# Kernel tuning notes

Measured on AMD Instinct MI355X. Metric: run time of the kernel, lower is better.

## Reference

```python
import jax, jax.numpy as jnp
import numpy as np

HYP_C = 0.1
TAU = 0.1
MRG = 0.1
CLIP_R = 2.3
BS = 1024
NB_PROXIES = 256
SZ_EMBED = 128
T_BATCH = BS * 50
T_LCA = NB_PROXIES * 50


@jax.custom_vjp
def artanh(x):
    xc = jnp.clip(x, -1.0 + 1e-5, 1.0 - 1e-5)
    return 0.5 * (jnp.log1p(xc) - jnp.log1p(-xc))

def _artanh_fwd(x):
    xc = jnp.clip(x, -1.0 + 1e-5, 1.0 - 1e-5)
    return 0.5 * (jnp.log1p(xc) - jnp.log1p(-xc)), xc

def _artanh_bwd(xc, g):
    return (g / (1.0 - xc * xc),)

artanh.defvjp(_artanh_fwd, _artanh_bwd)


@jax.custom_vjp
def riemannian_fix(x):
    # identity fwd; bwd rescales euclidean grad to riemannian grad on the ball
    return x

def _riem_fwd(x):
    return x, x

def _riem_bwd(x, g):
    scale = ((1.0 - HYP_C * jnp.sum(x * x, axis=-1, keepdims=True)) ** 2) / 4.0
    return (g * scale,)

riemannian_fix.defvjp(_riem_fwd, _riem_bwd)


def expmap0(x, c):
    sqrt_c = c ** 0.5
    xn = jnp.maximum(jnp.linalg.norm(x, axis=-1, keepdims=True), 1e-5)
    return jnp.tanh(sqrt_c * xn) * x / (sqrt_c * xn)


def project(x, c):
    norm = jnp.maximum(jnp.linalg.norm(x, axis=-1, keepdims=True), 1e-5)
    maxnorm = (1.0 - 1e-3) / (c ** 0.5)
    return jnp.where(norm > maxnorm, x / norm * maxnorm, x)


def to_poincare(x, c, clip_r):
    xn = jnp.linalg.norm(x, axis=-1, keepdims=True) + 1e-5
    x = x * jnp.minimum(jnp.ones_like(xn), clip_r / xn)
    return riemannian_fix(project(expmap0(x, c), c))


def dist_matrix(x, y, c):
    # ||mobius_add(-x, y)|| computed in closed form (same math as the [N,M,D]
    # num/denom construction in the torch code; num_{nm} = a*( -x_n ) + b*y_m).
    sqrt_c = c ** 0.5
    xy = -jnp.einsum('nd,md->nm', x, y)        # (-x) . y
    x2 = jnp.sum(x * x, axis=-1, keepdims=True)  # [N,1]
    y2t = jnp.sum(y * y, axis=-1)[None, :]       # [1,M]
    a = 1.0 + 2.0 * c * xy + c * y2t             # coeff of -x
    b = 1.0 - c * x2                             # coeff of y
    denom = 1.0 + 2.0 * c * xy + (c ** 2) * x2 * y2t
    num_sq = a * a * x2 + 2.0 * a * b * xy + b * b * y2t
    norm = jnp.sqrt(jnp.maximum(num_sq, 1e-12)) / jnp.abs(denom + 1e-5)
    return (2.0 / sqrt_c) * artanh(sqrt_c * norm)


def gumbel_softmax_hard(logits, g):
    # straight-through hard gumbel softmax (tau=1 as in F.gumbel_softmax default)
    y = jax.nn.softmax(logits + g, axis=-1)
    hard = jax.nn.one_hot(jnp.argmax(y, axis=-1), y.shape[-1], dtype=y.dtype)
    return y + jax.lax.stop_gradient(hard - y)


def compute_ghhc(cp_dist, trip, g):
    i, j, k = trip[0], trip[1], trip[2]
    di, dj, dk = cp_dist[i], cp_dist[j], cp_dist[k]   # [T,P] each
    max_ij = jnp.maximum(di, dj)
    p_ij = gumbel_softmax_hard(-max_ij / TAU, g[0])
    max_ijk = jnp.maximum(dk, max_ij)
    p_ijk = gumbel_softmax_hard(-max_ijk / TAU, g[1])
    diff_lca = (jnp.argmax(p_ij, -1) != jnp.argmax(p_ijk, -1)).astype(cp_dist.dtype)
    d_i_ij = jnp.sum(di * p_ij, axis=1)
    d_i_ijk = jnp.sum(di * p_ijk, axis=1)
    d_j_ij = jnp.sum(dj * p_ij, axis=1)
    d_j_ijk = jnp.sum(dj * p_ijk, axis=1)
    d_k_ij = jnp.sum(dk * p_ij, axis=1)
    d_k_ijk = jnp.sum(dk * p_ijk, axis=1)
    hc = (jax.nn.relu(d_i_ij - d_i_ijk + MRG)
          + jax.nn.relu(d_j_ij - d_j_ijk + MRG)
          + jax.nn.relu(d_k_ijk - d_k_ij + MRG))
    return jnp.mean(hc * diff_lca)


def hp_loss(z_s, t_s, lcas, trip1, trip2, trip3, trip4, g1, g2, g3, g4):
    bs = z_s.shape[0]
    lh = to_poincare(lcas, HYP_C, CLIP_R)
    all_nodes = jnp.concatenate([z_s, lh], axis=0)
    D = dist_matrix(all_nodes, all_nodes, HYP_C)
    t_all = jnp.concatenate([t_s, lh], axis=0)
    Dt = dist_matrix(t_all, t_all, HYP_C)
    loss = compute_ghhc(D[:bs, bs:], trip1, g1)
    loss = loss + compute_ghhc(D[bs:, bs:], trip2, g2)
    loss = loss + compute_ghhc(Dt[:bs, bs:], trip3, g3)
    loss = loss + compute_ghhc(Dt[bs:, bs:], trip4, g4)
    return loss


def setup_inputs() -> dict:
    key = jax.random.key(0)
    ks = jax.random.split(key, 12)
    z_s = jax.random.normal(ks[0], (BS, SZ_EMBED), dtype=jnp.float32)
    t_s = jax.random.normal(ks[1], (BS, SZ_EMBED), dtype=jnp.float32)
    y = jax.random.uniform(ks[2], (BS, 24), dtype=jnp.float32)
    # lcas param init: randn / sqrt(d) * clip_r * 0.9
    lcas = jax.random.normal(ks[3], (NB_PROXIES, SZ_EMBED), dtype=jnp.float32)
    lcas = lcas / np.sqrt(SZ_EMBED) * CLIP_R * 0.9
    trip1 = jax.random.randint(ks[4], (3, T_BATCH), 0, BS, dtype=jnp.int32)
    trip2 = jax.random.randint(ks[5], (3, T_LCA), 0, NB_PROXIES, dtype=jnp.int32)
    trip3 = jax.random.randint(ks[6], (3, T_BATCH), 0, BS, dtype=jnp.int32)
    trip4 = jax.random.randint(ks[7], (3, T_LCA), 0, NB_PROXIES, dtype=jnp.int32)
    g1 = jax.random.gumbel(ks[8], (2, T_BATCH, NB_PROXIES), dtype=jnp.float32)
    g2 = jax.random.gumbel(ks[9], (2, T_LCA, NB_PROXIES), dtype=jnp.float32)
    g3 = jax.random.gumbel(ks[10], (2, T_BATCH, NB_PROXIES), dtype=jnp.float32)
    g4 = jax.random.gumbel(ks[11], (2, T_LCA, NB_PROXIES), dtype=jnp.float32)
    return {"z_s": z_s, "t_s": t_s, "y": y, "lcas": lcas,
            "trip1": trip1, "trip2": trip2, "trip3": trip3, "trip4": trip4,
            "g1": g1, "g2": g2, "g3": g3, "g4": g4}


def reference(z_s, t_s, y, lcas, trip1, trip2, trip3, trip4, g1, g2, g3, g4):
    # y only feeds the detached numpy mining loop in the original; the mined
    # triplets are supplied precomputed (trip1..4), so y does not enter the math.
    return hp_loss(z_s, t_s, lcas, trip1, trip2, trip3, trip4, g1, g2, g3, g4)
```

## Files before the change

### kernel.cpp

```cpp
#include <hip/hip_runtime.h>
#include <cstddef>
#include <stdint.h>

#define HYP_C   0.1f
#define SQRT_C  0.31622776601683794f
#define CLIP_R  2.3f
#define MRG     0.1f
#define NPROX   256
#define DIM     128

#define OFF_LH   0
#define OFF_LHT  32768
#define OFF_LN2  65536
#define OFF_D1   65792
#define OFF_D2   327936
#define OFF_D3   393472

__global__ __launch_bounds__(128)
void to_poincare_kernel(const float* __restrict__ lcas,
                        float* __restrict__ ws,
                        float* __restrict__ out)
{
    const int row = blockIdx.x;
    const int k   = threadIdx.x;
    if (row == 0 && k == 0) out[0] = 0.0f;

    float v  = lcas[row * DIM + k];
    float ss = v * v;
    #pragma unroll
    for (int off = 32; off >= 1; off >>= 1)
        ss += __shfl_xor(ss, off, 64);
    __shared__ float wpart[2];
    if ((k & 63) == 0) wpart[k >> 6] = ss;
    __syncthreads();
    const float sumsq = wpart[0] + wpart[1];

    const float s1 = sqrtf(sumsq);
    const float xn = s1 + 1e-5f;
    const float f1 = fminf(1.0f, CLIP_R / xn);
    const float xn2 = fmaxf(f1 * s1, 1e-5f);
    const float th  = tanhf(SQRT_C * xn2);
    const float f2  = th / (SQRT_C * xn2);
    const float nr      = fmaxf(f2 * f1 * s1, 1e-5f);
    const float maxnorm = (1.0f - 1e-3f) / SQRT_C;
    const float f3      = (nr > maxnorm) ? (maxnorm / nr) : 1.0f;

    const float f  = f3 * f2 * f1;
    const float lv = f * v;
    ws[OFF_LH  + row * DIM + k]   = lv;
    ws[OFF_LHT + k * NPROX + row] = lv;
    if (k == 0) ws[OFF_LN2 + row] = f * f * sumsq;
}

__global__ __launch_bounds__(256)
void dist_all_kernel(const float* __restrict__ z,
                     const float* __restrict__ t,
                     float* __restrict__ ws, int nb1)
{
    const float* lhT = ws + OFF_LHT;
    const float* ln2 = ws + OFF_LN2;

    int b = blockIdx.x;
    const float* X; float* Dout; int row0;
    if (b < nb1)            { X = z;            Dout = ws + OFF_D1; row0 = b * 4; }
    else if (b < nb1 + 64)  { X = ws + OFF_LH;  Dout = ws + OFF_D2; row0 = (b - nb1) * 4; }
    else                    { X = t;            Dout = ws + OFF_D3; row0 = (b - nb1 - 64) * 4; }

    __shared__ float xs[4][DIM];
    __shared__ float sx2[4];

    for (int idx = threadIdx.x; idx < 4 * DIM; idx += 256)
        xs[idx / DIM][idx % DIM] = X[row0 * DIM + idx];
    __syncthreads();

    const int wid  = threadIdx.x >> 6;
    const int lane = threadIdx.x & 63;
    {
        float a = xs[wid][lane];
        float c = xs[wid][lane + 64];
        float s = a * a + c * c;
        #pragma unroll
        for (int off = 32; off >= 1; off >>= 1)
            s += __shfl_xor(s, off, 64);
        if (lane == 0) sx2[wid] = s;
    }
    __syncthreads();

    const int m = threadIdx.x;
    float dot0 = 0.f, dot1 = 0.f, dot2 = 0.f, dot3 = 0.f;
    #pragma unroll 8
    for (int k = 0; k < DIM; k += 4) {
        const float4 x0 = *(const float4*)&xs[0][k];
        const float4 x1 = *(const float4*)&xs[1][k];
        const float4 x2 = *(const float4*)&xs[2][k];
        const float4 x3 = *(const float4*)&xs[3][k];
        const float l0 = lhT[(k + 0) * NPROX + m];
        const float l1 = lhT[(k + 1) * NPROX + m];
        const float l2 = lhT[(k + 2) * NPROX + m];
        const float l3 = lhT[(k + 3) * NPROX + m];
        dot0 = fmaf(x0.x, l0, fmaf(x0.y, l1, fmaf(x0.z, l2, fmaf(x0.w, l3, dot0))));
        dot1 = fmaf(x1.x, l0, fmaf(x1.y, l1, fmaf(x1.z, l2, fmaf(x1.w, l3, dot1))));
        dot2 = fmaf(x2.x, l0, fmaf(x2.y, l1, fmaf(x2.z, l2, fmaf(x2.w, l3, dot2))));
        dot3 = fmaf(x3.x, l0, fmaf(x3.y, l1, fmaf(x3.z, l2, fmaf(x3.w, l3, dot3))));
    }

    const float y2 = ln2[m];
    float dots[4] = {dot0, dot1, dot2, dot3};
    #pragma unroll
    for (int r = 0; r < 4; ++r) {
        const float x2 = sx2[r];
        const float xy = -dots[r];
        const float a  = 1.0f + 2.0f * HYP_C * xy + HYP_C * y2;
        const float bb = 1.0f - HYP_C * x2;
        const float denom  = 1.0f + 2.0f * HYP_C * xy + HYP_C * HYP_C * x2 * y2;
        const float num_sq = a * a * x2 + 2.0f * a * bb * xy + bb * bb * y2;
        const float nrm = sqrtf(fmaxf(num_sq, 1e-12f)) / fabsf(denom + 1e-5f);
        float u = SQRT_C * nrm;
        u = fminf(fmaxf(u, -1.0f + 1e-5f), 1.0f - 1e-5f);
        const float d = (2.0f / SQRT_C) * (0.5f * (log1pf(u) - log1pf(-u)));
        Dout[(size_t)(row0 + r) * NPROX + m] = d;
    }
}

__device__ __forceinline__ float dpp_fmax16(float x) {
    int o;
    o = __builtin_amdgcn_update_dpp(0, __float_as_int(x), 0x121, 0xF, 0xF, true);
    x = fmaxf(x, __int_as_float(o));
    o = __builtin_amdgcn_update_dpp(0, __float_as_int(x), 0x122, 0xF, 0xF, true);
    x = fmaxf(x, __int_as_float(o));
    o = __builtin_amdgcn_update_dpp(0, __float_as_int(x), 0x124, 0xF, 0xF, true);
    x = fmaxf(x, __int_as_float(o));
    o = __builtin_amdgcn_update_dpp(0, __float_as_int(x), 0x128, 0xF, 0xF, true);
    x = fmaxf(x, __int_as_float(o));
    return x;
}

__device__ __forceinline__ int dpp_imin16(int x) {
    int o;
    o = __builtin_amdgcn_update_dpp(0, x, 0x121, 0xF, 0xF, true); x = min(x, o);
    o = __builtin_amdgcn_update_dpp(0, x, 0x122, 0xF, 0xF, true); x = min(x, o);
    o = __builtin_amdgcn_update_dpp(0, x, 0x124, 0xF, 0xF, true); x = min(x, o);
    o = __builtin_amdgcn_update_dpp(0, x, 0x128, 0xF, 0xF, true); x = min(x, o);
    return x;
}

__device__ __forceinline__ float wave_fmax(float x) {
    x = dpp_fmax16(x);
    x = fmaxf(x, __shfl_xor(x, 16, 64));
    x = fmaxf(x, __shfl_xor(x, 32, 64));
    return x;
}

__device__ __forceinline__ int wave_imin(int x) {
    x = dpp_imin16(x);
    x = min(x, __shfl_xor(x, 16, 64));
    x = min(x, __shfl_xor(x, 32, 64));
    return x;
}

__device__ __forceinline__ void ld_row_async(const float* src, const float* lds_dst, int lane) {
    typedef __attribute__((address_space(3))) uint32_t as3_u32;
    typedef const __attribute__((address_space(1))) uint32_t as1_u32;
    __builtin_amdgcn_global_load_lds((as1_u32*)(src + 4 * lane),
                                     (as3_u32*)(uint32_t)(uintptr_t)lds_dst,
                                     16, 0, 0);
}

__device__ __forceinline__ float sel4(const float4 v, int c) {
    const float lo = (c & 1) ? v.y : v.x;
    const float hi = (c & 1) ? v.w : v.z;
    return (c & 2) ? hi : lo;
}

__global__ __launch_bounds__(256)
void ghhc_fused_kernel(const float* __restrict__ Da, const float* __restrict__ Db,
                       const float* __restrict__ Dc, const float* __restrict__ Dd,
                       const int* __restrict__ ta, const int* __restrict__ tb,
                       const int* __restrict__ tc, const int* __restrict__ td,
                       const float* __restrict__ ga, const float* __restrict__ gb,
                       const float* __restrict__ gc, const float* __restrict__ gd,
                       int Ta, int Tb, int Tc, int Td,
                       float sa, float sb, float sc_, float sd,
                       int nba, int nbb, int nbc,
                       float* __restrict__ out)
{
    const int tid  = threadIdx.x;
    const int w    = tid >> 6;
    const int lane = tid & 63;

    const int b = blockIdx.x;
    const float* D; const int* tr; const float* g; int Tt; float sc; int lb;
    if (b < nba)                   { D = Da; tr = ta; g = ga; Tt = Ta; sc = sa;  lb = b; }
    else if (b < nba + nbb)        { D = Db; tr = tb; g = gb; Tt = Tb; sc = sb;  lb = b - nba; }
    else if (b < nba + nbb + nbc)  { D = Dc; tr = tc; g = gc; Tt = Tc; sc = sc_; lb = b - nba - nbb; }
    else                           { D = Dd; tr = td; g = gd; Tt = Td; sc = sd;  lb = b - nba - nbb - nbc; }

    const int tstart = lb * 64 + w * 16;

    int tl = tstart + (lane & 15);
    tl = (tl < Tt) ? tl : (Tt - 1);
    const int idxi = tr[tl];
    const int idxj = tr[Tt + tl];
    const int idxk = tr[2 * Tt + tl];

    __shared__ float sbuf[4 * 2 * 5 * 256];
    float* const wbase = sbuf + w * 2560;

    #define ISSUE(IT) { \
        const int t_  = tstart + (IT); \
        const int te_ = (t_ < Tt) ? t_ : (Tt - 1); \
        const int i_  = __shfl(idxi, (IT) & 15, 64); \
        const int j_  = __shfl(idxj, (IT) & 15, 64); \
        const int k_  = __shfl(idxk, (IT) & 15, 64); \
        float* B_ = wbase + ((IT) & 1) * 1280; \
        ld_row_async(D + (size_t)i_ * NPROX,          B_ +    0, lane); \
        ld_row_async(D + (size_t)j_ * NPROX,          B_ +  256, lane); \
        ld_row_async(D + (size_t)k_ * NPROX,          B_ +  512, lane); \
        ld_row_async(g + (size_t)te_ * NPROX,         B_ +  768, lane); \
        ld_row_async(g + ((size_t)Tt + te_) * NPROX,  B_ + 1024, lane); \
    }

    float acc = 0.0f;

    ISSUE(0); ISSUE(1);

    #define STEP(IT) { \
        if ((IT) == 15) { asm volatile("s_waitcnt vmcnt(0)" ::: "memory"); } \
        else            { asm volatile("s_waitcnt vmcnt(5)" ::: "memory"); } \
        __builtin_amdgcn_sched_barrier(0); \
        const float* B_ = wbase + ((IT) & 1) * 1280; \
        const float4 di = ((const float4*)(B_ +    0))[lane]; \
        const float4 dj = ((const float4*)(B_ +  256))[lane]; \
        const float4 dk = ((const float4*)(B_ +  512))[lane]; \
        const float4 q0 = ((const float4*)(B_ +  768))[lane]; \
        const float4 q1 = ((const float4*)(B_ + 1024))[lane]; \
        float S0, S1, S2, S3, U0, U1, U2, U3; \
        { float m1, m2; \
          m1 = fmaxf(di.x, dj.x); S0 = fmaf(m1, -10.0f, q0.x); m2 = fmaxf(dk.x, m1); U0 = fmaf(m2, -10.0f, q1.x); \
          m1 = fmaxf(di.y, dj.y); S1 = fmaf(m1, -10.0f, q0.y); m2 = fmaxf(dk.y, m1); U1 = fmaf(m2, -10.0f, q1.y); \
          m1 = fmaxf(di.z, dj.z); S2 = fmaf(m1, -10.0f, q0.z); m2 = fmaxf(dk.z, m1); U2 = fmaf(m2, -10.0f, q1.z); \
          m1 = fmaxf(di.w, dj.w); S3 = fmaf(m1, -10.0f, q0.w); m2 = fmaxf(dk.w, m1); U3 = fmaf(m2, -10.0f, q1.w); } \
        __builtin_amdgcn_sched_barrier(0); \
        if ((IT) + 2 < 16) ISSUE((IT) + 2) \
        const float gvA = wave_fmax(fmaxf(fmaxf(S0, S1), fmaxf(S2, S3))); \
        const float gvB = wave_fmax(fmaxf(fmaxf(U0, U1), fmaxf(U2, U3))); \
        int slA = 4, slB = 4; \
        slA = (S3 == gvA) ? 3 : slA; slA = (S2 == gvA) ? 2 : slA; \
        slA = (S1 == gvA) ? 1 : slA; slA = (S0 == gvA) ? 0 : slA; \
        slB = (U3 == gvB) ? 3 : slB; slB = (U2 == gvB) ? 2 : slB; \
        slB = (U1 == gvB) ? 1 : slB; slB = (U0 == gvB) ? 0 : slB; \
        const int eA = (slA < 4) ? ((lane << 2) | slA) : 1024; \
        const int eB = (slB < 4) ? ((lane << 2) | slB) : 1024; \
        const int Ag = wave_imin(eA); \
        const int Bg = wave_imin(eB); \
        const int lA = Ag >> 2, cA = Ag & 3; \
        const int lB = Bg >> 2, cB = Bg & 3; \
        const float diA = __shfl(sel4(di, cA), lA, 64); \
        const float djA = __shfl(sel4(dj, cA), lA, 64); \
        const float dkA = __shfl(sel4(dk, cA), lA, 64); \
        const float diB = __shfl(sel4(di, cB), lB, 64); \
        const float djB = __shfl(sel4(dj, cB), lB, 64); \
        const float dkB = __shfl(sel4(dk, cB), lB, 64); \
        const float hc = fmaxf(diA - diB + MRG, 0.0f) \
                       + fmaxf(djA - djB + MRG, 0.0f) \
                       + fmaxf(dkB - dkA + MRG, 0.0f); \
        acc += (((tstart + (IT)) < Tt) && (Ag != Bg) && lane == 0) ? hc * sc : 0.0f; \
    }

    STEP(0)  STEP(1)  STEP(2)  STEP(3)
    STEP(4)  STEP(5)  STEP(6)  STEP(7)
    STEP(8)  STEP(9)  STEP(10) STEP(11)
    STEP(12) STEP(13) STEP(14) STEP(15)

    #undef STEP
    #undef ISSUE

    if (lane == 0) wbase[0] = acc;
    __syncthreads();
    if (tid == 0)
        atomicAdd(out, sbuf[0] + sbuf[2560] + sbuf[5120] + sbuf[7680]);
}

extern "C" void kernel_launch(void* const* d_in, const int* in_sizes, int n_in,
                              void* d_out, int out_size, void* d_ws, size_t ws_size,
                              hipStream_t stream)
{
    const float* z_s  = (const float*)d_in[0];
    const float* t_s  = (const float*)d_in[1];
    const float* lcas = (const float*)d_in[3];
    const int* trip1 = (const int*)d_in[4];
    const int* trip2 = (const int*)d_in[5];
    const int* trip3 = (const int*)d_in[6];
    const int* trip4 = (const int*)d_in[7];
    const float* g1 = (const float*)d_in[8];
    const float* g2 = (const float*)d_in[9];
    const float* g3 = (const float*)d_in[10];
    const float* g4 = (const float*)d_in[11];
    float* out = (float*)d_out;
    float* ws  = (float*)d_ws;

    const int T1 = in_sizes[4] / 3;
    const int T2 = in_sizes[5] / 3;
    const int T3 = in_sizes[6] / 3;
    const int T4 = in_sizes[7] / 3;
    const int BS = in_sizes[0] / DIM;
    const int nb1 = BS / 4;

    to_poincare_kernel<<<NPROX, 128, 0, stream>>>(lcas, ws, out);

    dist_all_kernel<<<2 * nb1 + 64, 256, 0, stream>>>(z_s, t_s, ws, nb1);

    const int nbA = (T1 + 63) / 64;
    const int nbB = (T2 + 63) / 64;
    const int nbC = (T3 + 63) / 64;
    const int nbD = (T4 + 63) / 64;
    ghhc_fused_kernel<<<nbA + nbB + nbC + nbD, 256, 0, stream>>>(
        ws + OFF_D1, ws + OFF_D2, ws + OFF_D3, ws + OFF_D2,
        trip1, trip2, trip3, trip4,
        g1, g2, g3, g4,
        T1, T2, T3, T4,
        1.0f / (float)T1, 1.0f / (float)T2, 1.0f / (float)T3, 1.0f / (float)T4,
        nbA, nbB, nbC,
        out);
}
```

Baseline: 305.1 us.

## Load distance rows into registers and deepen gumbel prefetch pipeline

Distance-matrix rows are now loaded straight into registers through a three-deep rotating float4 buffer, and only the gumbel rows still go through async global-to-LDS copies. Those copies now use a four-slot ring prefetched three steps ahead, with per-step vmcnt wait counts tuned to match. This removes the LDS round trip for the gathered D rows, raises the number of loads in flight, and shrinks shared memory per block. In exchange it uses more registers, and the hand-set waitcnt values must exactly match the order loads are issued in.

```diff
diff --git a/kernel.cpp b/kernel.cpp
--- a/kernel.cpp
+++ b/kernel.cpp
@@ -203,45 +203,55 @@
     const int idxj = tr[Tt + tl];
     const int idxk = tr[2 * Tt + tl];
 
-    __shared__ float sbuf[4 * 2 * 5 * 256];
-    float* const wbase = sbuf + w * 2560;
-
-    #define ISSUE(IT) { \
+    __shared__ __align__(16) float sbuf[4 * 4 * 512];
+    float* const wbase = sbuf + w * 2048;
+
+    float4 bdi[3], bdj[3], bdk[3];
+
+    #define ISSUE_D(IT) { \
+        const int i_ = __shfl(idxi, (IT) & 15, 64); \
+        const int j_ = __shfl(idxj, (IT) & 15, 64); \
+        const int k_ = __shfl(idxk, (IT) & 15, 64); \
+        bdi[(IT) % 3] = ((const float4*)(D + (size_t)i_ * NPROX))[lane]; \
+        bdj[(IT) % 3] = ((const float4*)(D + (size_t)j_ * NPROX))[lane]; \
+        bdk[(IT) % 3] = ((const float4*)(D + (size_t)k_ * NPROX))[lane]; \
+    }
+
+    #define ISSUE_G(IT) { \
         const int t_  = tstart + (IT); \
         const int te_ = (t_ < Tt) ? t_ : (Tt - 1); \
-        const int i_  = __shfl(idxi, (IT) & 15, 64); \
-        const int j_  = __shfl(idxj, (IT) & 15, 64); \
-        const int k_  = __shfl(idxk, (IT) & 15, 64); \
-        float* B_ = wbase + ((IT) & 1) * 1280; \
-        ld_row_async(D + (size_t)i_ * NPROX,          B_ +    0, lane); \
-        ld_row_async(D + (size_t)j_ * NPROX,          B_ +  256, lane); \
-        ld_row_async(D + (size_t)k_ * NPROX,          B_ +  512, lane); \
-        ld_row_async(g + (size_t)te_ * NPROX,         B_ +  768, lane); \
-        ld_row_async(g + ((size_t)Tt + te_) * NPROX,  B_ + 1024, lane); \
+        float* B_ = wbase + ((IT) % 4) * 512; \
+        ld_row_async(g + (size_t)te_ * NPROX,         B_ +   0, lane); \
+        ld_row_async(g + ((size_t)Tt + te_) * NPROX,  B_ + 256, lane); \
     }
 
     float acc = 0.0f;
 
-    ISSUE(0); ISSUE(1);
-
-    #define STEP(IT) { \
-        if ((IT) == 15) { asm volatile("s_waitcnt vmcnt(0)" ::: "memory"); } \
-        else            { asm volatile("s_waitcnt vmcnt(5)" ::: "memory"); } \
+    ISSUE_G(0); ISSUE_G(1); ISSUE_G(2);
+    __builtin_amdgcn_sched_barrier(0);
+    ISSUE_D(0);
+    __builtin_amdgcn_sched_barrier(0);
+    ISSUE_D(1);
+    __builtin_amdgcn_sched_barrier(0);
+
+    #define STEP(IT, VM) { \
+        if ((IT) + 2 < 16) ISSUE_D((IT) + 2) \
         __builtin_amdgcn_sched_barrier(0); \
-        const float* B_ = wbase + ((IT) & 1) * 1280; \
-        const float4 di = ((const float4*)(B_ +    0))[lane]; \
-        const float4 dj = ((const float4*)(B_ +  256))[lane]; \
-        const float4 dk = ((const float4*)(B_ +  512))[lane]; \
-        const float4 q0 = ((const float4*)(B_ +  768))[lane]; \
-        const float4 q1 = ((const float4*)(B_ + 1024))[lane]; \
+        if ((IT) + 3 < 16) ISSUE_G((IT) + 3) \
+        asm volatile("s_waitcnt vmcnt(" VM ")" ::: "memory"); \
+        __builtin_amdgcn_sched_barrier(0); \
+        const float* B_ = wbase + ((IT) % 4) * 512; \
+        const float4 q0 = ((const float4*)(B_ +   0))[lane]; \
+        const float4 q1 = ((const float4*)(B_ + 256))[lane]; \
+        const float4 di = bdi[(IT) % 3]; \
+        const float4 dj = bdj[(IT) % 3]; \
+        const float4 dk = bdk[(IT) % 3]; \
         float S0, S1, S2, S3, U0, U1, U2, U3; \
         { float m1, m2; \
           m1 = fmaxf(di.x, dj.x); S0 = fmaf(m1, -10.0f, q0.x); m2 = fmaxf(dk.x, m1); U0 = fmaf(m2, -10.0f, q1.x); \
           m1 = fmaxf(di.y, dj.y); S1 = fmaf(m1, -10.0f, q0.y); m2 = fmaxf(dk.y, m1); U1 = fmaf(m2, -10.0f, q1.y); \
           m1 = fmaxf(di.z, dj.z); S2 = fmaf(m1, -10.0f, q0.z); m2 = fmaxf(dk.z, m1); U2 = fmaf(m2, -10.0f, q1.z); \
           m1 = fmaxf(di.w, dj.w); S3 = fmaf(m1, -10.0f, q0.w); m2 = fmaxf(dk.w, m1); U3 = fmaf(m2, -10.0f, q1.w); } \
-        __builtin_amdgcn_sched_barrier(0); \
-        if ((IT) + 2 < 16) ISSUE((IT) + 2) \
         const float gvA = wave_fmax(fmaxf(fmaxf(S0, S1), fmaxf(S2, S3))); \
         const float gvB = wave_fmax(fmaxf(fmaxf(U0, U1), fmaxf(U2, U3))); \
         int slA = 4, slB = 4; \
@@ -267,18 +277,19 @@
         acc += (((tstart + (IT)) < Tt) && (Ag != Bg) && lane == 0) ? hc * sc : 0.0f; \
     }
 
-    STEP(0)  STEP(1)  STEP(2)  STEP(3)
-    STEP(4)  STEP(5)  STEP(6)  STEP(7)
-    STEP(8)  STEP(9)  STEP(10) STEP(11)
-    STEP(12) STEP(13) STEP(14) STEP(15)
+    STEP(0,"8")   STEP(1,"10")  STEP(2,"12")  STEP(3,"12")
+    STEP(4,"12")  STEP(5,"12")  STEP(6,"12")  STEP(7,"12")
+    STEP(8,"12")  STEP(9,"12")  STEP(10,"12") STEP(11,"12")
+    STEP(12,"12") STEP(13,"10") STEP(14,"5")  STEP(15,"0")
 
     #undef STEP
-    #undef ISSUE
+    #undef ISSUE_D
+    #undef ISSUE_G
 
     if (lane == 0) wbase[0] = acc;
     __syncthreads();
     if (tid == 0)
-        atomicAdd(out, sbuf[0] + sbuf[2560] + sbuf[5120] + sbuf[7680]);
+        atomicAdd(out, sbuf[0] + sbuf[2048] + sbuf[4096] + sbuf[6144]);
 }
 
 extern "C" void kernel_launch(void* const* d_in, const int* in_sizes, int n_in,
```

Result: no change. 304.9 us (-0.1%).
